# Optimization experiments

Hardware: AMD Instinct MI355X
Metric: run time of the kernel (lower is better)

## Reference

```python
import jax, jax.numpy as jnp
import numpy as np

IN_FEATURES = 1024
ACT_BITS = 4


def _hadamard(size: int) -> np.ndarray:
    # Sylvester construction, normalized: H(n) = Sylvester(n) / sqrt(n)
    h = np.array([[1.0]], dtype=np.float64)
    while h.shape[0] < size:
        h = np.block([[h, h], [h, -h]])
    return (h / np.sqrt(size)).astype(np.float32)


def _quantize_activations(x, bits=ACT_BITS):
    pos = 2 ** (bits - 1) - 1  # 7
    neg = 2 ** (bits - 1)      # 8
    scale = jnp.clip(jnp.max(jnp.abs(jax.lax.stop_gradient(x)), axis=-1, keepdims=True), 1e-5) / pos
    q = jnp.clip(jnp.round(x / scale), -neg, pos) * scale
    return x + jax.lax.stop_gradient(q - x)  # STE


def _ternary_quantize_ste(w):
    scale = jnp.clip(jnp.mean(jnp.abs(jax.lax.stop_gradient(w)), axis=1, keepdims=True), 1e-5)
    n = w / scale
    tern = jnp.where(n > 0.5, 1.0, jnp.where(n < -0.5, -1.0, 0.0))
    q = tern * scale
    return w + jax.lax.stop_gradient(q - w)  # STE


def setup_inputs() -> dict:
    key = jax.random.key(0)
    k1, k2 = jax.random.split(key)
    x = jax.random.normal(k1, (8, 8192, IN_FEATURES), dtype=jnp.float32)
    # master weight ~ kaiming-uniform-ish scale
    bound = 1.0 / np.sqrt(IN_FEATURES)
    weight = jax.random.uniform(k2, (1024, IN_FEATURES), dtype=jnp.float32, minval=-bound, maxval=bound)
    return {"x": x, "weight": weight}


def reference(x, weight):
    H = jnp.asarray(_hadamard(IN_FEATURES))  # [in, in]
    xh = x @ H                                # Hadamard precondition on input
    xq = _quantize_activations(xh)            # per-token 4-bit symmetric quant (STE)
    wq = _ternary_quantize_ste(weight)        # per-row ternary quant (STE)
    return jnp.einsum('bsi,oi->bso', xq, wq)  # F.linear, no bias
```

## Files before the change

kernel.cpp:

```cpp
#include <hip/hip_runtime.h>
#include <stdint.h>

typedef int v4i __attribute__((ext_vector_type(4)));
typedef float float4_t __attribute__((ext_vector_type(4)));

#define K_DIM 1024
#define N_DIM 1024
#define BM 128
#define BN 128

__device__ __forceinline__ void gload16(const void* g, void* l) {
  __builtin_amdgcn_global_load_lds(
      (const __attribute__((address_space(1))) unsigned int*)g,
      (__attribute__((address_space(3))) unsigned int*)l, 16, 0, 0);
}

#define MFMA_I8 __builtin_amdgcn_mfma_i32_16x16x64_i8

__global__ __launch_bounds__(256) void fwht_quant_kernel(
    const float* __restrict__ x, int8_t* __restrict__ qx,
    float* __restrict__ ascale, int M) {
  const int lane = threadIdx.x & 63;
  const int wid = threadIdx.x >> 6;
  const long token = (long)blockIdx.x * 4 + wid;
  if (token >= M) return;
  const float4_t* xr4 = (const float4_t*)(x + token * K_DIM);

  float v[16];
#pragma unroll
  for (int i = 0; i < 4; ++i) {
    float4_t f = xr4[lane * 4 + i];
#pragma unroll
    for (int c = 0; c < 4; ++c) v[i * 4 + c] = f[c];
  }
#pragma unroll
  for (int s = 1; s <= 8; s <<= 1) {
#pragma unroll
    for (int r = 0; r < 16; ++r)
      if ((r & s) == 0) {
        float a0 = v[r], b0 = v[r | s];
        v[r] = a0 + b0;
        v[r | s] = a0 - b0;
      }
  }
#pragma unroll
  for (int m = 1; m <= 32; m <<= 1) {
    const float sg = (lane & m) ? -1.0f : 1.0f;
#pragma unroll
    for (int r = 0; r < 16; ++r) {
      float p = __shfl_xor(v[r], m, 64);
      v[r] = fmaf(sg, v[r], p);
    }
  }
  float mx = 0.f;
#pragma unroll
  for (int r = 0; r < 16; ++r) mx = fmaxf(mx, fabsf(v[r]));
#pragma unroll
  for (int m = 32; m >= 1; m >>= 1) mx = fmaxf(mx, __shfl_xor(mx, m, 64));
  const float scale = fmaxf(mx * 0.03125f, 1e-5f) * (1.0f / 7.0f);
  if (lane == 0) ascale[token] = scale;
  const float inv = 0.03125f / scale;

  v4i pk;
#pragma unroll
  for (int i = 0; i < 4; ++i) {
    int packed = 0;
#pragma unroll
    for (int c = 0; c < 4; ++c) {
      float q = rintf(v[i * 4 + c] * inv);
      q = fminf(7.f, fmaxf(-8.f, q));
      packed |= ((int)q & 0xff) << (8 * c);
    }
    pk[i] = packed;
  }
  *(v4i*)(qx + token * K_DIM + lane * 16) = pk;
}

__global__ __launch_bounds__(256) void wquant_kernel(
    const float* __restrict__ w, int8_t* __restrict__ qw,
    float* __restrict__ wscale) {
  const int lane = threadIdx.x & 63;
  const int wid = threadIdx.x >> 6;
  const int row = blockIdx.x * 4 + wid;
  const float* wr = w + (long)row * K_DIM;

  float v[16];
  float s = 0.f;
  const float4_t* wr4 = (const float4_t*)wr;
#pragma unroll
  for (int rr = 0; rr < 4; ++rr) {
    float4_t f = wr4[rr * 64 + lane];
#pragma unroll
    for (int c = 0; c < 4; ++c) {
      v[rr * 4 + c] = f[c];
      s += fabsf(f[c]);
    }
  }
#pragma unroll
  for (int m = 32; m >= 1; m >>= 1) s += __shfl_xor(s, m, 64);
  const float scale = fmaxf(s * (1.0f / 1024.0f), 1e-5f);
  if (lane == 0) wscale[row] = scale;

  int8_t* qr = qw + (long)row * K_DIM;
#pragma unroll
  for (int rr = 0; rr < 4; ++rr) {
    int packed = 0;
#pragma unroll
    for (int c = 0; c < 4; ++c) {
      float n = v[rr * 4 + c] / scale;
      int t = (n > 0.5f) ? 1 : ((n < -0.5f) ? -1 : 0);
      packed |= (t & 0xff) << (8 * c);
    }
    *(int*)(qr + rr * 256 + lane * 4) = packed;
  }
}

__global__ __launch_bounds__(256) void gemm_i8_kernel(
    const int8_t* __restrict__ A, const int8_t* __restrict__ B,
    const float* __restrict__ asc, const float* __restrict__ wsc,
    float* __restrict__ C, int M) {
  __shared__ __align__(16) int8_t smem[2][32768];
  float* tr = (float*)smem;

  const int t = threadIdx.x;
  const int lane = t & 63;
  const int wm = (t >> 6) >> 1;
  const int wn = (t >> 6) & 1;
  const int rl = lane & 15;
  const int kb = lane >> 4;

  const int swz = ((int)blockIdx.x & 7) * 512 + ((int)blockIdx.x >> 3);
  const long bm = swz >> 3;
  const int bn = swz & 7;

  const int chunkoff = (((t & 7) ^ ((t >> 3) & 7)) << 4);
  const int8_t* gA = A + (bm * BM + (t >> 3)) * (long)K_DIM + chunkoff;
  const int8_t* gB = B + ((long)bn * BN + (t >> 3)) * K_DIM + chunkoff;

  const int sw0 = ((kb ^ (rl & 7)) << 4);
  const int sw1 = (((4 + kb) ^ (rl & 7)) << 4);
  const int arow = (wm * 64 + rl) * 128;
  const int brow = (wn * 64 + rl) * 128;

  v4i acc[4][4] = {};

#define STAGE(p, ks)                                      \
  gload16(gA + (ks), smem[p] + t * 16);                   \
  gload16(gA + (ks) + 32 * K_DIM, smem[p] + 4096 + t * 16);  \
  gload16(gA + (ks) + 64 * K_DIM, smem[p] + 8192 + t * 16);  \
  gload16(gA + (ks) + 96 * K_DIM, smem[p] + 12288 + t * 16); \
  gload16(gB + (ks), smem[p] + 16384 + t * 16);              \
  gload16(gB + (ks) + 32 * K_DIM, smem[p] + 20480 + t * 16); \
  gload16(gB + (ks) + 64 * K_DIM, smem[p] + 24576 + t * 16); \
  gload16(gB + (ks) + 96 * K_DIM, smem[p] + 28672 + t * 16);

  STAGE(0, 0);
  __syncthreads();

#pragma unroll
  for (int kt = 0; kt < 8; ++kt) {
    const int p = kt & 1;
    if (kt < 7) {
      STAGE(p ^ 1, (kt + 1) * 128);
    }
    const int8_t* Al = smem[p];
    const int8_t* Bl = smem[p] + 16384;
#pragma unroll
    for (int ks2 = 0; ks2 < 2; ++ks2) {
      const int sw = ks2 ? sw1 : sw0;
      v4i a[4], b[4];
#pragma unroll
      for (int i = 0; i < 4; ++i)
        a[i] = *(const v4i*)(Al + arow + i * 2048 + sw);
#pragma unroll
      for (int j = 0; j < 4; ++j)
        b[j] = *(const v4i*)(Bl + brow + j * 2048 + sw);
#pragma unroll
      for (int i = 0; i < 4; ++i)
#pragma unroll
        for (int j = 0; j < 4; ++j)
          acc[i][j] = MFMA_I8(a[i], b[j], acc[i][j], 0, 0, 0);
    }
    __syncthreads();
  }
#undef STAGE

  const long rowg0 = bm * BM + wm * 64;
  const int colg0 = bn * BN + wn * 64;
#pragma unroll
  for (int c = 0; c < 2; ++c) {
    if (wm == c) {
#pragma unroll
      for (int i = 0; i < 4; ++i) {
        float as[4];
#pragma unroll
        for (int r = 0; r < 4; ++r) as[r] = asc[rowg0 + i * 16 + kb * 4 + r];
#pragma unroll
        for (int j = 0; j < 4; ++j) {
          const float ws = wsc[colg0 + j * 16 + rl];
#pragma unroll
          for (int r = 0; r < 4; ++r)
            tr[(i * 16 + kb * 4 + r) * 132 + wn * 64 + j * 16 + rl] =
                (float)acc[i][j][r] * as[r] * ws;
        }
      }
    }
    __syncthreads();
#pragma unroll
    for (int it = 0; it < 8; ++it) {
      const int idx = t + it * 256;
      const int rl2 = idx >> 5;
      const int c4 = (idx & 31) * 4;
      const float4_t val = *(const float4_t*)(tr + rl2 * 132 + c4);
      __builtin_nontemporal_store(
          val, (float4_t*)(C + (bm * BM + c * 64 + rl2) * (long)N_DIM + bn * BN + c4));
    }
    __syncthreads();
  }
}

extern "C" void kernel_launch(void* const* d_in, const int* in_sizes, int n_in,
                              void* d_out, int out_size, void* d_ws, size_t ws_size,
                              hipStream_t stream) {
  const float* x = (const float*)d_in[0];
  const float* w = (const float*)d_in[1];
  float* out = (float*)d_out;
  const int M = in_sizes[0] / K_DIM;

  int8_t* qx = (int8_t*)d_ws;
  int8_t* qw = qx + (size_t)M * K_DIM;
  float* ascale = (float*)(qw + (size_t)N_DIM * K_DIM);
  float* wscale = ascale + M;

  fwht_quant_kernel<<<(M + 3) / 4, 256, 0, stream>>>(x, qx, ascale, M);
  wquant_kernel<<<N_DIM / 4, 256, 0, stream>>>(w, qw, wscale);
  gemm_i8_kernel<<<(M / BM) * (N_DIM / BN), 256, 0, stream>>>(qx, qw, ascale, wscale, out, M);
}
```

Measured before the change: 167.3 us.

## Triple-buffer A tiles and use partial vmcnt waits in int8 GEMM

Splits the shared staging buffer into a three-stage ring for the activation tile and a two-stage ring for the weight tile, so activation loads are issued two K-steps ahead. The full __syncthreads at the end of each iteration becomes an explicit s_waitcnt vmcnt(4) plus s_barrier, letting the newest A prefetch stay in flight across the barrier. The redundant final barrier in the epilogue is also dropped. LDS use grows from 64 KB to 80 KB, which could limit resident blocks, and the hand-counted vmcnt values tie correctness to the exact load count per stage.

Measured after the change: 169.9 us. Within noise of the previous version (+1.5%).

```diff
diff --git a/kernel.cpp b/kernel.cpp
--- a/kernel.cpp
+++ b/kernel.cpp
@@ -119,8 +119,9 @@
     const int8_t* __restrict__ A, const int8_t* __restrict__ B,
     const float* __restrict__ asc, const float* __restrict__ wsc,
     float* __restrict__ C, int M) {
-  __shared__ __align__(16) int8_t smem[2][32768];
-  float* tr = (float*)smem;
+  __shared__ __align__(16) int8_t Abuf[3][16384];
+  __shared__ __align__(16) int8_t Bbuf[2][16384];
+  float* tr = (float*)Abuf;
 
   const int t = threadIdx.x;
   const int lane = t & 63;
@@ -144,27 +145,37 @@
 
   v4i acc[4][4] = {};
 
-#define STAGE(p, ks)                                      \
-  gload16(gA + (ks), smem[p] + t * 16);                   \
-  gload16(gA + (ks) + 32 * K_DIM, smem[p] + 4096 + t * 16);  \
-  gload16(gA + (ks) + 64 * K_DIM, smem[p] + 8192 + t * 16);  \
-  gload16(gA + (ks) + 96 * K_DIM, smem[p] + 12288 + t * 16); \
-  gload16(gB + (ks), smem[p] + 16384 + t * 16);              \
-  gload16(gB + (ks) + 32 * K_DIM, smem[p] + 20480 + t * 16); \
-  gload16(gB + (ks) + 64 * K_DIM, smem[p] + 24576 + t * 16); \
-  gload16(gB + (ks) + 96 * K_DIM, smem[p] + 28672 + t * 16);
-
-  STAGE(0, 0);
-  __syncthreads();
+#define STAGE_A(p, ks)                                     \
+  gload16(gA + (ks), Abuf[p] + t * 16);                    \
+  gload16(gA + (ks) + 32 * K_DIM, Abuf[p] + 4096 + t * 16); \
+  gload16(gA + (ks) + 64 * K_DIM, Abuf[p] + 8192 + t * 16); \
+  gload16(gA + (ks) + 96 * K_DIM, Abuf[p] + 12288 + t * 16);
+#define STAGE_B(p, ks)                                     \
+  gload16(gB + (ks), Bbuf[p] + t * 16);                    \
+  gload16(gB + (ks) + 32 * K_DIM, Bbuf[p] + 4096 + t * 16); \
+  gload16(gB + (ks) + 64 * K_DIM, Bbuf[p] + 8192 + t * 16); \
+  gload16(gB + (ks) + 96 * K_DIM, Bbuf[p] + 12288 + t * 16);
+
+  STAGE_A(0, 0);
+  STAGE_B(0, 0);
+  STAGE_A(1, 128);
+  asm volatile("s_waitcnt vmcnt(4)" ::: "memory");
+  asm volatile("s_barrier" ::: "memory");
 
 #pragma unroll
   for (int kt = 0; kt < 8; ++kt) {
-    const int p = kt & 1;
+    const int p3 = kt % 3;
+    const int p2 = kt & 1;
+    const int8_t* Al = Abuf[p3];
+    const int8_t* Bl = Bbuf[p2];
+
     if (kt < 7) {
-      STAGE(p ^ 1, (kt + 1) * 128);
-    }
-    const int8_t* Al = smem[p];
-    const int8_t* Bl = smem[p] + 16384;
+      STAGE_B((kt + 1) & 1, (kt + 1) * 128);
+    }
+    if (kt < 6) {
+      STAGE_A((kt + 2) % 3, (kt + 2) * 128);
+    }
+
 #pragma unroll
     for (int ks2 = 0; ks2 < 2; ++ks2) {
       const int sw = ks2 ? sw1 : sw0;
@@ -181,9 +192,19 @@
         for (int j = 0; j < 4; ++j)
           acc[i][j] = MFMA_I8(a[i], b[j], acc[i][j], 0, 0, 0);
     }
-    __syncthreads();
-  }
-#undef STAGE
+
+    if (kt < 6) {
+      asm volatile("s_waitcnt vmcnt(4)" ::: "memory");
+      asm volatile("s_barrier" ::: "memory");
+    } else if (kt == 6) {
+      asm volatile("s_waitcnt vmcnt(0)" ::: "memory");
+      asm volatile("s_barrier" ::: "memory");
+    }
+  }
+#undef STAGE_A
+#undef STAGE_B
+
+  __syncthreads();
 
   const long rowg0 = bm * BM + wm * 64;
   const int colg0 = bn * BN + wn * 64;
@@ -215,7 +236,7 @@
       __builtin_nontemporal_store(
           val, (float4_t*)(C + (bm * BM + c * 64 + rl2) * (long)N_DIM + bn * BN + c4));
     }
-    __syncthreads();
+    if (c == 0) __syncthreads();
   }
 }
 
```
